# Optimization experiments

Hardware: AMD Instinct MI355X
Metric: run time of the kernel (lower is better)

The kernel has to match this reference:

```python
import jax, jax.numpy as jnp
import numpy as np

INPUT_DIMS = 512
OUTPUT_DIMS = 512
DEGREE = 7
ALPHA = 1.0


def setup_inputs() -> dict:
    key = jax.random.key(0)
    k1, k2 = jax.random.split(key)
    x = jax.random.normal(k1, (16384, INPUT_DIMS), dtype=jnp.float32)
    std = 1.0 / (INPUT_DIMS * (DEGREE + 1))
    coeffs = jax.random.normal(k2, (INPUT_DIMS, OUTPUT_DIMS, DEGREE + 1), dtype=jnp.float32) * std
    return {"x": x, "gegenbauer_coeffs": coeffs}


def reference(x, gegenbauer_coeffs):
    # x: (B, I) -> tanh squashed into (-1, 1) domain of Gegenbauer polys
    x = jnp.tanh(x.reshape(-1, INPUT_DIMS))
    a = ALPHA
    polys = [jnp.ones_like(x)]
    if DEGREE > 0:
        polys.append(2.0 * a * x)
    # recurrence: C_{n+1} = (2(n+a) x C_n - (n+2a-1) C_{n-1}) / (n+1)
    for n in range(1, DEGREE):
        polys.append((2.0 * (n + a) * x * polys[n] - (n + 2.0 * a - 1.0) * polys[n - 1]) / (n + 1.0))
    g = jnp.stack(polys, axis=-1)  # (B, I, D+1)
    y = jnp.einsum('bid,iod->bo', g, gegenbauer_coeffs)
    return y.reshape(-1, OUTPUT_DIMS)
```

## Files before the change

kernel.cpp:

```cpp
#include <hip/hip_runtime.h>
#include <hip/hip_bf16.h>


#define I_DIM 512
#define O_DIM 512
#define NDEG 8
#define KH_ITERS 32
#define W_ELEMS (I_DIM * O_DIM * NDEG)

typedef __attribute__((ext_vector_type(8))) short s8v;
typedef __attribute__((ext_vector_type(4))) float f32x4;
typedef unsigned short u16;

__device__ __forceinline__ unsigned cvt_pk_bf16(float lo, float hi) {
    unsigned r;
    asm("v_cvt_pk_bf16_f32 %0, %1, %2" : "=v"(r) : "v"(lo), "v"(hi));
    return r;
}

__device__ __forceinline__ float fast_tanh(float v) {
    float e = __expf(v + v);
    float r = __builtin_amdgcn_rcpf(e + 1.0f);
    return 1.0f - (r + r);
}

__device__ __forceinline__ s8v feat_frag(float xv) {
    const float t  = fast_tanh(xv);
    const float t2 = t + t;
    const float c1 = t2;
    const float c2 = t2 * c1 - 1.0f;
    const float c3 = t2 * c2 - c1;
    const float c4 = t2 * c3 - c2;
    const float c5 = t2 * c4 - c3;
    const float c6 = t2 * c5 - c4;
    const float c7 = t2 * c6 - c5;
    union { s8v s; unsigned u[4]; } pk;
    pk.u[0] = cvt_pk_bf16(1.0f, c1);
    pk.u[1] = cvt_pk_bf16(c2, c3);
    pk.u[2] = cvt_pk_bf16(c4, c5);
    pk.u[3] = cvt_pk_bf16(c6, c7);
    return pk.s;
}

extern "C" __global__ __launch_bounds__(256)
void cvt_w(const float* __restrict__ cf, u16* __restrict__ wbf) {
    const size_t idx = ((size_t)blockIdx.x * 256 + threadIdx.x) * 4;
    const float4 v = *reinterpret_cast<const float4*>(cf + idx);
    unsigned* dst = reinterpret_cast<unsigned*>(wbf + idx);
    dst[0] = cvt_pk_bf16(v.x, v.y);
    dst[1] = cvt_pk_bf16(v.z, v.w);
}

template <bool PRECONV>
__global__ __launch_bounds__(256, 2)
void gegen_gemm(const float* __restrict__ x,
                const float* __restrict__ cf,
                const u16* __restrict__ wbf,
                float* __restrict__ out)
{
    __shared__ float smem[4096];

    const int tid  = threadIdx.x;
    const int lane = tid & 63;
    const int wave = tid >> 6;
    const int m4   = wave & 1;
    const int kh   = wave >> 1;
    const int fm   = lane & 15;
    const int fq   = lane >> 4;

    const int bm0 = blockIdx.x * 128 + m4 * 64;
    const int bn0 = blockIdx.y * 128;

    const float* xrow = x + (size_t)(bm0 + lane) * I_DIM;
    float* xslot = &smem[wave * 1024];

    f32x4 acc[4][8];
#pragma unroll
    for (int a = 0; a < 4; ++a)
#pragma unroll
        for (int b = 0; b < 8; ++b)
            acc[a][b] = (f32x4){0.0f, 0.0f, 0.0f, 0.0f};

    for (int it = 0; it < KH_ITERS; ++it) {
        const int g8  = (kh * KH_ITERS + it) * 8;
        const int buf = (it & 1) * 512;

        const float4 xa = *reinterpret_cast<const float4*>(xrow + g8);
        const float4 xb = *reinterpret_cast<const float4*>(xrow + g8 + 4);

        s8v bfr0[8], bfr1[8];
        if (PRECONV) {
            const u16* wb0 = wbf + ((size_t)(g8 + fq) * O_DIM + bn0 + fm) * NDEG;
            const u16* wb1 = wb0 + (size_t)4 * O_DIM * NDEG;
#pragma unroll
            for (int tn = 0; tn < 8; ++tn)
                bfr0[tn] = *reinterpret_cast<const s8v*>(wb0 + tn * 16 * NDEG);
#pragma unroll
            for (int tn = 0; tn < 8; ++tn)
                bfr1[tn] = *reinterpret_cast<const s8v*>(wb1 + tn * 16 * NDEG);
        } else {
            const float* wb0 = cf + ((size_t)(g8 + fq) * O_DIM + bn0 + fm) * NDEG;
            const float* wb1 = wb0 + (size_t)4 * O_DIM * NDEG;
#pragma unroll
            for (int tn = 0; tn < 8; ++tn) {
                const float4 w0 = reinterpret_cast<const float4*>(wb0 + tn * 16 * NDEG)[0];
                const float4 w1 = reinterpret_cast<const float4*>(wb0 + tn * 16 * NDEG)[1];
                union { s8v s; unsigned u[4]; } pk;
                pk.u[0] = cvt_pk_bf16(w0.x, w0.y);
                pk.u[1] = cvt_pk_bf16(w0.z, w0.w);
                pk.u[2] = cvt_pk_bf16(w1.x, w1.y);
                pk.u[3] = cvt_pk_bf16(w1.z, w1.w);
                bfr0[tn] = pk.s;
            }
#pragma unroll
            for (int tn = 0; tn < 8; ++tn) {
                const float4 w0 = reinterpret_cast<const float4*>(wb1 + tn * 16 * NDEG)[0];
                const float4 w1 = reinterpret_cast<const float4*>(wb1 + tn * 16 * NDEG)[1];
                union { s8v s; unsigned u[4]; } pk;
                pk.u[0] = cvt_pk_bf16(w0.x, w0.y);
                pk.u[1] = cvt_pk_bf16(w0.z, w0.w);
                pk.u[2] = cvt_pk_bf16(w1.x, w1.y);
                pk.u[3] = cvt_pk_bf16(w1.z, w1.w);
                bfr1[tn] = pk.s;
            }
        }

        *reinterpret_cast<f32x4*>(&xslot[buf + lane * 8])     = (f32x4){xa.x, xa.y, xa.z, xa.w};
        *reinterpret_cast<f32x4*>(&xslot[buf + lane * 8 + 4]) = (f32x4){xb.x, xb.y, xb.z, xb.w};
        asm volatile("s_waitcnt lgkmcnt(0)" ::: "memory");
        __builtin_amdgcn_sched_barrier(0);

        s8v afr0[4], afr1[4];
#pragma unroll
        for (int tm = 0; tm < 4; ++tm) {
            const float xv0 = xslot[buf + (tm * 16 + fm) * 8 + fq];
            const float xv1 = xslot[buf + (tm * 16 + fm) * 8 + 4 + fq];
            afr0[tm] = feat_frag(xv0);
            afr1[tm] = feat_frag(xv1);
        }

#pragma unroll
        for (int tm = 0; tm < 4; ++tm)
#pragma unroll
            for (int tn = 0; tn < 8; ++tn)
                acc[tm][tn] = __builtin_amdgcn_mfma_f32_16x16x32_bf16(
                    afr0[tm], bfr0[tn], acc[tm][tn], 0, 0, 0);
#pragma unroll
        for (int tm = 0; tm < 4; ++tm)
#pragma unroll
            for (int tn = 0; tn < 8; ++tn)
                acc[tm][tn] = __builtin_amdgcn_mfma_f32_16x16x32_bf16(
                    afr1[tm], bfr1[tn], acc[tm][tn], 0, 0, 0);
    }

    __syncthreads();
#pragma unroll
    for (int tm = 0; tm < 4; ++tm) {
        if (kh == 1) {
#pragma unroll
            for (int tn = 0; tn < 8; ++tn)
#pragma unroll
                for (int r = 0; r < 4; ++r)
                    smem[m4 * 2048 + (fq * 4 + r) * 128 + tn * 16 + fm] = acc[tm][tn][r];
        }
        __syncthreads();
        if (kh == 0) {
#pragma unroll
            for (int tn = 0; tn < 8; ++tn) {
                const int row = bm0 + tm * 16 + fq * 4;
                const int col = bn0 + tn * 16 + fm;
#pragma unroll
                for (int r = 0; r < 4; ++r)
                    out[(size_t)(row + r) * O_DIM + col] =
                        acc[tm][tn][r] + smem[m4 * 2048 + (fq * 4 + r) * 128 + tn * 16 + fm];
            }
        }
        __syncthreads();
    }
}

extern "C" void kernel_launch(void* const* d_in, const int* in_sizes, int n_in,
                              void* d_out, int out_size, void* d_ws, size_t ws_size,
                              hipStream_t stream) {
    const float* x  = (const float*)d_in[0];
    const float* cf = (const float*)d_in[1];
    float* out = (float*)d_out;
    const int M = in_sizes[0] / I_DIM;
    dim3 grid(M / 128, O_DIM / 128);
    dim3 block(256, 1, 1);

    if (ws_size >= (size_t)W_ELEMS * sizeof(u16)) {
        u16* wbf = (u16*)d_ws;
        cvt_w<<<W_ELEMS / 1024, 256, 0, stream>>>(cf, wbf);
        gegen_gemm<true><<<grid, block, 0, stream>>>(x, cf, wbf, out);
    } else {
        gegen_gemm<false><<<grid, block, 0, stream>>>(x, cf, nullptr, out);
    }
}
```

Before: 153.0 us.

## Load x directly into registers with one-iteration prefetch, drop LDS staging

Each lane now loads the x scalars its MFMA fragments need straight from global memory, which removes the LDS round-trip and the lgkmcnt wait. The loads for the next iteration are issued a step early. Feature computation is split into two halves interleaved with the MFMA groups, which lowers register pressure, and the MFMA blocks are wrapped in s_setprio to favour matrix issue. The trade-off is scalar, strided global loads in place of coalesced float4 loads. The __syncthreads before the epilogue is also removed, which matters because smem is still reused for the reduction.

```diff
diff --git a/kernel.cpp b/kernel.cpp
--- a/kernel.cpp
+++ b/kernel.cpp
@@ -70,9 +70,12 @@
 
     const int bm0 = blockIdx.x * 128 + m4 * 64;
     const int bn0 = blockIdx.y * 128;
-
-    const float* xrow = x + (size_t)(bm0 + lane) * I_DIM;
-    float* xslot = &smem[wave * 1024];
+    const int kbase = kh * (KH_ITERS * 8);
+
+    const float* xg0 = x + (size_t)(bm0 +  0 + fm) * I_DIM + kbase + fq;
+    const float* xg1 = x + (size_t)(bm0 + 16 + fm) * I_DIM + kbase + fq;
+    const float* xg2 = x + (size_t)(bm0 + 32 + fm) * I_DIM + kbase + fq;
+    const float* xg3 = x + (size_t)(bm0 + 48 + fm) * I_DIM + kbase + fq;
 
     f32x4 acc[4][8];
 #pragma unroll
@@ -81,12 +84,14 @@
         for (int b = 0; b < 8; ++b)
             acc[a][b] = (f32x4){0.0f, 0.0f, 0.0f, 0.0f};
 
+    float xc[8], xn[8];
+    xc[0] = xg0[0]; xc[1] = xg0[4];
+    xc[2] = xg1[0]; xc[3] = xg1[4];
+    xc[4] = xg2[0]; xc[5] = xg2[4];
+    xc[6] = xg3[0]; xc[7] = xg3[4];
+
     for (int it = 0; it < KH_ITERS; ++it) {
-        const int g8  = (kh * KH_ITERS + it) * 8;
-        const int buf = (it & 1) * 512;
-
-        const float4 xa = *reinterpret_cast<const float4*>(xrow + g8);
-        const float4 xb = *reinterpret_cast<const float4*>(xrow + g8 + 4);
+        const int g8 = kbase + it * 8;
 
         s8v bfr0[8], bfr1[8];
         if (PRECONV) {
@@ -125,35 +130,43 @@
             }
         }
 
-        *reinterpret_cast<f32x4*>(&xslot[buf + lane * 8])     = (f32x4){xa.x, xa.y, xa.z, xa.w};
-        *reinterpret_cast<f32x4*>(&xslot[buf + lane * 8 + 4]) = (f32x4){xb.x, xb.y, xb.z, xb.w};
-        asm volatile("s_waitcnt lgkmcnt(0)" ::: "memory");
-        __builtin_amdgcn_sched_barrier(0);
-
-        s8v afr0[4], afr1[4];
-#pragma unroll
-        for (int tm = 0; tm < 4; ++tm) {
-            const float xv0 = xslot[buf + (tm * 16 + fm) * 8 + fq];
-            const float xv1 = xslot[buf + (tm * 16 + fm) * 8 + 4 + fq];
-            afr0[tm] = feat_frag(xv0);
-            afr1[tm] = feat_frag(xv1);
-        }
-
+        const int off = (it + 1 < KH_ITERS ? it + 1 : it) * 8;
+        xn[0] = xg0[off]; xn[1] = xg0[off + 4];
+        xn[2] = xg1[off]; xn[3] = xg1[off + 4];
+        xn[4] = xg2[off]; xn[5] = xg2[off + 4];
+        xn[6] = xg3[off]; xn[7] = xg3[off + 4];
+
+        s8v afr[4];
+        afr[0] = feat_frag(xc[0]);
+        afr[1] = feat_frag(xc[2]);
+        afr[2] = feat_frag(xc[4]);
+        afr[3] = feat_frag(xc[6]);
+        __builtin_amdgcn_s_setprio(1);
 #pragma unroll
         for (int tm = 0; tm < 4; ++tm)
 #pragma unroll
             for (int tn = 0; tn < 8; ++tn)
                 acc[tm][tn] = __builtin_amdgcn_mfma_f32_16x16x32_bf16(
-                    afr0[tm], bfr0[tn], acc[tm][tn], 0, 0, 0);
+                    afr[tm], bfr0[tn], acc[tm][tn], 0, 0, 0);
+        __builtin_amdgcn_s_setprio(0);
+
+        afr[0] = feat_frag(xc[1]);
+        afr[1] = feat_frag(xc[3]);
+        afr[2] = feat_frag(xc[5]);
+        afr[3] = feat_frag(xc[7]);
+        __builtin_amdgcn_s_setprio(1);
 #pragma unroll
         for (int tm = 0; tm < 4; ++tm)
 #pragma unroll
             for (int tn = 0; tn < 8; ++tn)
                 acc[tm][tn] = __builtin_amdgcn_mfma_f32_16x16x32_bf16(
-                    afr1[tm], bfr1[tn], acc[tm][tn], 0, 0, 0);
+                    afr[tm], bfr1[tn], acc[tm][tn], 0, 0, 0);
+        __builtin_amdgcn_s_setprio(0);
+
+#pragma unroll
+        for (int e = 0; e < 8; ++e) xc[e] = xn[e];
     }
 
-    __syncthreads();
 #pragma unroll
     for (int tm = 0; tm < 4; ++tm) {
         if (kh == 1) {
```

After: 179.1 us. +17.1%, slower.

## Prefetch next x tile into double buffer and interleave feature compute with MFMA

Applied to the files above, without the earlier changes.

Loads the next iteration's x values into registers early and writes them into the alternate LDS buffer after the MFMAs, so the global load latency overlaps compute. Computes feature fragments in two halves, each followed by its MFMA block, which reduces live registers and lets VALU work overlap the matrix ops. Raises wave priority around the MFMA blocks with s_setprio. The sched_barrier is removed, and the software pipeline adds register pressure from the prefetched values.

```diff
diff --git a/kernel.cpp b/kernel.cpp
--- a/kernel.cpp
+++ b/kernel.cpp
@@ -70,8 +70,9 @@
 
     const int bm0 = blockIdx.x * 128 + m4 * 64;
     const int bn0 = blockIdx.y * 128;
-
-    const float* xrow = x + (size_t)(bm0 + lane) * I_DIM;
+    const int kbase = kh * (KH_ITERS * 8);
+
+    const float* xrow = x + (size_t)(bm0 + lane) * I_DIM + kbase;
     float* xslot = &smem[wave * 1024];
 
     f32x4 acc[4][8];
@@ -81,12 +82,17 @@
         for (int b = 0; b < 8; ++b)
             acc[a][b] = (f32x4){0.0f, 0.0f, 0.0f, 0.0f};
 
+    {
+        const float4 xa = *reinterpret_cast<const float4*>(xrow);
+        const float4 xb = *reinterpret_cast<const float4*>(xrow + 4);
+        *reinterpret_cast<f32x4*>(&xslot[lane * 8])     = (f32x4){xa.x, xa.y, xa.z, xa.w};
+        *reinterpret_cast<f32x4*>(&xslot[lane * 8 + 4]) = (f32x4){xb.x, xb.y, xb.z, xb.w};
+    }
+
     for (int it = 0; it < KH_ITERS; ++it) {
-        const int g8  = (kh * KH_ITERS + it) * 8;
-        const int buf = (it & 1) * 512;
-
-        const float4 xa = *reinterpret_cast<const float4*>(xrow + g8);
-        const float4 xb = *reinterpret_cast<const float4*>(xrow + g8 + 4);
+        const int g8   = kbase + it * 8;
+        const int buf  = (it & 1) * 512;
+        const int nbuf = buf ^ 512;
 
         s8v bfr0[8], bfr1[8];
         if (PRECONV) {
@@ -125,32 +131,46 @@
             }
         }
 
-        *reinterpret_cast<f32x4*>(&xslot[buf + lane * 8])     = (f32x4){xa.x, xa.y, xa.z, xa.w};
-        *reinterpret_cast<f32x4*>(&xslot[buf + lane * 8 + 4]) = (f32x4){xb.x, xb.y, xb.z, xb.w};
+        float4 xa2, xb2;
+        const bool more = (it + 1 < KH_ITERS);
+        if (more) {
+            xa2 = *reinterpret_cast<const float4*>(xrow + (it + 1) * 8);
+            xb2 = *reinterpret_cast<const float4*>(xrow + (it + 1) * 8 + 4);
+        }
+
         asm volatile("s_waitcnt lgkmcnt(0)" ::: "memory");
-        __builtin_amdgcn_sched_barrier(0);
-
-        s8v afr0[4], afr1[4];
-#pragma unroll
-        for (int tm = 0; tm < 4; ++tm) {
-            const float xv0 = xslot[buf + (tm * 16 + fm) * 8 + fq];
-            const float xv1 = xslot[buf + (tm * 16 + fm) * 8 + 4 + fq];
-            afr0[tm] = feat_frag(xv0);
-            afr1[tm] = feat_frag(xv1);
-        }
-
+
+        s8v afr[4];
+#pragma unroll
+        for (int tm = 0; tm < 4; ++tm)
+            afr[tm] = feat_frag(xslot[buf + (tm * 16 + fm) * 8 + fq]);
+
+        __builtin_amdgcn_s_setprio(1);
 #pragma unroll
         for (int tm = 0; tm < 4; ++tm)
 #pragma unroll
             for (int tn = 0; tn < 8; ++tn)
                 acc[tm][tn] = __builtin_amdgcn_mfma_f32_16x16x32_bf16(
-                    afr0[tm], bfr0[tn], acc[tm][tn], 0, 0, 0);
+                    afr[tm], bfr0[tn], acc[tm][tn], 0, 0, 0);
+        __builtin_amdgcn_s_setprio(0);
+
+#pragma unroll
+        for (int tm = 0; tm < 4; ++tm)
+            afr[tm] = feat_frag(xslot[buf + (tm * 16 + fm) * 8 + 4 + fq]);
+
+        __builtin_amdgcn_s_setprio(1);
 #pragma unroll
         for (int tm = 0; tm < 4; ++tm)
 #pragma unroll
             for (int tn = 0; tn < 8; ++tn)
                 acc[tm][tn] = __builtin_amdgcn_mfma_f32_16x16x32_bf16(
-                    afr1[tm], bfr1[tn], acc[tm][tn], 0, 0, 0);
+                    afr[tm], bfr1[tn], acc[tm][tn], 0, 0, 0);
+        __builtin_amdgcn_s_setprio(0);
+
+        if (more) {
+            *reinterpret_cast<f32x4*>(&xslot[nbuf + lane * 8])     = (f32x4){xa2.x, xa2.y, xa2.z, xa2.w};
+            *reinterpret_cast<f32x4*>(&xslot[nbuf + lane * 8 + 4]) = (f32x4){xb2.x, xb2.y, xb2.z, xb2.w};
+        }
     }
 
     __syncthreads();
```

After: 153.9 us. No clear change (+0.6%).
